# Performance work log

Measured on AMD Instinct MI355X. Metric: run time of the kernel, lower is better.

## Reference

```python
import jax, jax.numpy as jnp
import numpy as np

B, S, H, UNITS = 32, 2048, 1024, 1024


def setup_inputs() -> dict:
    key = jax.random.key(0)
    ks = jax.random.split(key, 5)
    scale = 1.0 / np.sqrt(H)
    return {
        "query": jax.random.normal(ks[0], (B, H), dtype=jnp.float32),
        "values": jax.random.normal(ks[1], (B, S, H), dtype=jnp.float32),
        "W1": jax.random.normal(ks[2], (H, UNITS), dtype=jnp.float32) * scale,
        "b1": jnp.zeros((UNITS,), dtype=jnp.float32),
        "W2": jax.random.normal(ks[3], (H, UNITS), dtype=jnp.float32) * scale,
        "b2": jnp.zeros((UNITS,), dtype=jnp.float32),
        "V": jax.random.normal(ks[4], (UNITS, 1), dtype=jnp.float32) * (1.0 / np.sqrt(UNITS)),
        "bV": jnp.zeros((1,), dtype=jnp.float32),
    }


def reference(query, values, W1, b1, W2, b2, V, bV):
    # W1(values): [B,S,U]; W2(query): [B,1,U] broadcast over S
    proj_v = jnp.einsum("bsh,hu->bsu", values, W1) + b1
    proj_q = (query @ W2 + b2)[:, None, :]
    score = jnp.tanh(proj_v + proj_q) @ V + bV          # [B,S,1]
    attention_weights = jax.nn.softmax(score, axis=1)   # softmax over seq
    context_vector = jnp.sum(attention_weights * values, axis=1)  # [B,H]
    return (attention_weights, context_vector)
```

## Files before the change

kernel.cpp:

```cpp
#include <hip/hip_runtime.h>
#include <hip/hip_bf16.h>
#include <stdint.h>

#define B_ 32
#define S_ 2048
#define H_ 1024
#define U_ 1024

typedef __attribute__((ext_vector_type(8))) short short8;
typedef __attribute__((ext_vector_type(4))) float f32x4;

__device__ __forceinline__ unsigned short f2bf(float f) {
  unsigned int u = __float_as_uint(f);
  u += 0x7fffu + ((u >> 16) & 1u);
  return (unsigned short)(u >> 16);
}

__global__ void k_transpose_w1(const float* __restrict__ W1, unsigned short* __restrict__ W1T) {
  __shared__ float tile[64][65];
  const int tx = threadIdx.x, ty = threadIdx.y;
  const int u0 = blockIdx.x * 64, h0 = blockIdx.y * 64;
#pragma unroll
  for (int i = 0; i < 16; ++i) {
    int hl = ty + i * 4;
    tile[hl][tx] = W1[(size_t)(h0 + hl) * U_ + (u0 + tx)];
  }
  __syncthreads();
#pragma unroll
  for (int i = 0; i < 16; ++i) {
    int ul = ty + i * 4;
    W1T[(size_t)(u0 + ul) * H_ + (h0 + tx)] = f2bf(tile[tx][ul]);
  }
}

__global__ void k_b1q(const float* __restrict__ query, const float* __restrict__ W2,
                      const float* __restrict__ b1, const float* __restrict__ b2,
                      float* __restrict__ b1q) {
  const int b = blockIdx.y;
  const int u = blockIdx.x * 256 + threadIdx.x;
  float acc = b1[u] + b2[u];
  const float* q = query + b * H_;
#pragma unroll 8
  for (int h = 0; h < H_; ++h) acc += q[h] * W2[(size_t)h * U_ + u];
  b1q[b * U_ + u] = acc;
}

#define BM 128
#define BN 512
#define BK 32
#define NT (H_ / BK)

__global__ __launch_bounds__(512, 2)
void k_fused_score(const float* __restrict__ values, const unsigned short* __restrict__ W1T,
                   const float* __restrict__ b1q, const float* __restrict__ V,
                   float* __restrict__ score_part) {
  __shared__ __align__(16) unsigned char smem[81920];
  unsigned short* As = (unsigned short*)smem;
  unsigned short* Bs = (unsigned short*)(smem + 16384);
  float* scorebuf = (float*)smem;

  const int tid = threadIdx.x;
  const int swz = blockIdx.x;
  const int seq = (swz & 7) * 128 + (swz >> 3);
  const int bn = seq & 1;
  const int bm = seq >> 1;

  const int lane = tid & 63, wid = tid >> 6;
  const int wm = wid >> 2, wn = wid & 3;

  const int arow = tid >> 2, aq = tid & 3;
  const float* aptr = values + (size_t)(bm * BM + arow) * H_ + aq * 8;
  const int awoff = arow * 32 + ((aq ^ ((arow >> 1) & 3)) << 3);

  const int bq = (lane & 3) ^ ((lane >> 3) & 3);
  const int u0 = bn * BN;

  const int fsq = (((lane >> 4) ^ ((lane >> 1) & 3)) << 3);

  f32x4 acc[4][8];
#pragma unroll
  for (int mf = 0; mf < 4; ++mf)
#pragma unroll
    for (int nf = 0; nf < 8; ++nf) acc[mf][nf] = (f32x4){0.f, 0.f, 0.f, 0.f};

  {
    const float4* p = (const float4*)aptr;
    float4 av0 = p[0], av1 = p[1];
#pragma unroll
    for (int i = 0; i < 4; ++i) {
      const int n = (wid * 4 + i) * 16 + (lane >> 2);
      const unsigned short* src = W1T + (size_t)(u0 + n) * H_ + bq * 8;
      __builtin_amdgcn_global_load_lds((const __attribute__((address_space(1))) void*)src,
                                       (__attribute__((address_space(3))) void*)&Bs[(wid * 4 + i) * 512],
                                       16, 0, 0);
    }
    short8 w;
    w[0]=f2bf(av0.x); w[1]=f2bf(av0.y); w[2]=f2bf(av0.z); w[3]=f2bf(av0.w);
    w[4]=f2bf(av1.x); w[5]=f2bf(av1.y); w[6]=f2bf(av1.z); w[7]=f2bf(av1.w);
    *(short8*)&As[awoff] = w;
  }
  __syncthreads();

  int cur = 0;
  for (int kt = 0; kt < NT; ++kt) {
    const bool more = (kt + 1 < NT);
    float4 av0, av1;
    if (more) {
      const float4* p = (const float4*)(aptr + (kt + 1) * BK);
      av0 = p[0]; av1 = p[1];
#pragma unroll
      for (int i = 0; i < 4; ++i) {
        const int n = (wid * 4 + i) * 16 + (lane >> 2);
        const unsigned short* src = W1T + (size_t)(u0 + n) * H_ + (kt + 1) * BK + bq * 8;
        __builtin_amdgcn_global_load_lds((const __attribute__((address_space(1))) void*)src,
                                         (__attribute__((address_space(3))) void*)&Bs[(cur ^ 1) * 16384 + (wid * 4 + i) * 512],
                                         16, 0, 0);
      }
    }
    short8 af[4], bfr[8];
#pragma unroll
    for (int mf = 0; mf < 4; ++mf) {
      const int row = wm * 64 + mf * 16 + (lane & 15);
      af[mf] = *(const short8*)&As[cur * 4096 + row * 32 + fsq];
    }
#pragma unroll
    for (int nf = 0; nf < 8; ++nf) {
      const int n = wn * 128 + nf * 16 + (lane & 15);
      bfr[nf] = *(const short8*)&Bs[cur * 16384 + n * 32 + fsq];
    }
#pragma unroll
    for (int nf = 0; nf < 8; ++nf)
#pragma unroll
      for (int mf = 0; mf < 4; ++mf)
        acc[mf][nf] = __builtin_amdgcn_mfma_f32_16x16x32_bf16(af[mf], bfr[nf], acc[mf][nf], 0, 0, 0);
    if (more) {
      short8 w;
      w[0]=f2bf(av0.x); w[1]=f2bf(av0.y); w[2]=f2bf(av0.z); w[3]=f2bf(av0.w);
      w[4]=f2bf(av1.x); w[5]=f2bf(av1.y); w[6]=f2bf(av1.z); w[7]=f2bf(av1.w);
      *(short8*)&As[(cur ^ 1) * 4096 + awoff] = w;
    }
    __syncthreads();
    cur ^= 1;
  }

  const int b_blk = bm >> 4;
  float bqv[8], vv[8];
#pragma unroll
  for (int nf = 0; nf < 8; ++nf) {
    const int ug = u0 + wn * 128 + nf * 16 + (lane & 15);
    bqv[nf] = b1q[b_blk * U_ + ug];
    vv[nf] = V[ug];
  }
  float rp[4][4];
#pragma unroll
  for (int mf = 0; mf < 4; ++mf)
#pragma unroll
    for (int j = 0; j < 4; ++j) rp[mf][j] = 0.f;
#pragma unroll
  for (int nf = 0; nf < 8; ++nf)
#pragma unroll
    for (int mf = 0; mf < 4; ++mf) {
      const f32x4 c = acc[mf][nf];
#pragma unroll
      for (int j = 0; j < 4; ++j) {
        const float x = c[j] + bqv[nf];
        const float e = __expf(2.f * x);
        const float t = 1.f - 2.f / (e + 1.f);
        rp[mf][j] += t * vv[nf];
      }
    }
#pragma unroll
  for (int mf = 0; mf < 4; ++mf)
#pragma unroll
    for (int j = 0; j < 4; ++j) {
      float v = rp[mf][j];
      v += __shfl_xor(v, 1);
      v += __shfl_xor(v, 2);
      v += __shfl_xor(v, 4);
      v += __shfl_xor(v, 8);
      rp[mf][j] = v;
    }
  if ((lane & 15) == 0) {
#pragma unroll
    for (int mf = 0; mf < 4; ++mf)
#pragma unroll
      for (int j = 0; j < 4; ++j)
        scorebuf[(wm * 64 + mf * 16 + (lane >> 4) * 4 + j) * 4 + wn] = rp[mf][j];
  }
  __syncthreads();
  if (tid < BM) {
    const float s = scorebuf[tid * 4 + 0] + scorebuf[tid * 4 + 1] +
                    scorebuf[tid * 4 + 2] + scorebuf[tid * 4 + 3];
    score_part[(size_t)bn * (B_ * S_) + bm * BM + tid] = s;
  }
}

__global__ void k_softmax(const float* __restrict__ p0, const float* __restrict__ p1,
                          float* __restrict__ aw) {
  __shared__ float red[8];
  const int b = blockIdx.x, tid = threadIdx.x;
  float x[8];
  float m = -1e30f;
#pragma unroll
  for (int i = 0; i < 8; ++i) {
    const int s = tid + i * 256;
    x[i] = p0[b * S_ + s] + p1[b * S_ + s];
    m = fmaxf(m, x[i]);
  }
#pragma unroll
  for (int off = 32; off; off >>= 1) m = fmaxf(m, __shfl_xor(m, off));
  if ((tid & 63) == 0) red[tid >> 6] = m;
  __syncthreads();
  m = fmaxf(fmaxf(red[0], red[1]), fmaxf(red[2], red[3]));
  float e[8];
  float sum = 0.f;
#pragma unroll
  for (int i = 0; i < 8; ++i) { e[i] = __expf(x[i] - m); sum += e[i]; }
#pragma unroll
  for (int off = 32; off; off >>= 1) sum += __shfl_xor(sum, off);
  __syncthreads();
  if ((tid & 63) == 0) red[4 + (tid >> 6)] = sum;
  __syncthreads();
  sum = red[4] + red[5] + red[6] + red[7];
  const float inv = 1.f / sum;
#pragma unroll
  for (int i = 0; i < 8; ++i) aw[b * S_ + tid + i * 256] = e[i] * inv;
}

__global__ void k_ctx_partial(const float* __restrict__ values, const float* __restrict__ aw,
                              float* __restrict__ part) {
  __shared__ float a_s[128];
  const int b = blockIdx.y, sc = blockIdx.x, tid = threadIdx.x;
  if (tid < 128) a_s[tid] = aw[b * S_ + sc * 128 + tid];
  __syncthreads();
  const float4* vp = (const float4*)values + (size_t)(b * S_ + sc * 128) * (H_ / 4) + tid;
  float4 acc = {0.f, 0.f, 0.f, 0.f};
#pragma unroll 4
  for (int i = 0; i < 128; ++i) {
    const float4 v = vp[(size_t)i * (H_ / 4)];
    const float a = a_s[i];
    acc.x += a * v.x; acc.y += a * v.y; acc.z += a * v.z; acc.w += a * v.w;
  }
  ((float4*)part)[(size_t)(b * 16 + sc) * (H_ / 4) + tid] = acc;
}

__global__ void k_ctx_combine(const float* __restrict__ part, float* __restrict__ ctx) {
  const int b = blockIdx.x, tid = threadIdx.x;
  float4 s = {0.f, 0.f, 0.f, 0.f};
#pragma unroll
  for (int c = 0; c < 16; ++c) {
    const float4 v = ((const float4*)part)[(size_t)(b * 16 + c) * (H_ / 4) + tid];
    s.x += v.x; s.y += v.y; s.z += v.z; s.w += v.w;
  }
  ((float4*)ctx)[b * (H_ / 4) + tid] = s;
}

extern "C" void kernel_launch(void* const* d_in, const int* in_sizes, int n_in,
                              void* d_out, int out_size, void* d_ws, size_t ws_size,
                              hipStream_t stream) {
  const float* query  = (const float*)d_in[0];
  const float* values = (const float*)d_in[1];
  const float* W1     = (const float*)d_in[2];
  const float* b1     = (const float*)d_in[3];
  const float* W2     = (const float*)d_in[4];
  const float* b2     = (const float*)d_in[5];
  const float* V      = (const float*)d_in[6];

  char* ws = (char*)d_ws;
  unsigned short* W1T = (unsigned short*)ws;
  float* b1q   = (float*)(ws + 2u * 1024u * 1024u);
  float* spart = (float*)(ws + 2u * 1024u * 1024u + 128u * 1024u);
  float* cpart = (float*)(ws + 2u * 1024u * 1024u + 128u * 1024u + 512u * 1024u);

  float* aw  = (float*)d_out;
  float* ctx = aw + B_ * S_;

  hipLaunchKernelGGL(k_transpose_w1, dim3(16, 16), dim3(64, 4), 0, stream, W1, W1T);
  hipLaunchKernelGGL(k_b1q,          dim3(4, 32),  dim3(256),   0, stream, query, W2, b1, b2, b1q);
  hipLaunchKernelGGL(k_fused_score,  dim3(1024),   dim3(512),   0, stream, values, W1T, b1q, V, spart);
  hipLaunchKernelGGL(k_softmax,      dim3(32),     dim3(256),   0, stream, spart, spart + B_ * S_, aw);
  hipLaunchKernelGGL(k_ctx_partial,  dim3(16, 32), dim3(256),   0, stream, values, aw, cpart);
  hipLaunchKernelGGL(k_ctx_combine,  dim3(32),     dim3(256),   0, stream, cpart, ctx);
}
```

Measured before the change: 314.1 us.

## Rewrite fused score GEMM with 256x256x64 tiles and explicit phased pipeline

The fused score GEMM moves from 128x512x32 tiles to 256x256 tiles with K=64, and the main loop is split into four phases per tile. Each phase uses manual vmcnt/lgkmcnt waits, sched barriers, raw s_barrier and setprio to overlap global loads, bf16 conversion into LDS and MFMA issue. A new XOR swizzle is applied to the LDS layout for both operands. Because there are now four N-partitions, softmax sums four score partials, which raises redundant fp32 A reads and workspace use. LDS grows to 128KB, so the launch_bounds(512,2) target may no longer be met, reducing occupancy.

```diff
diff --git a/kernel.cpp b/kernel.cpp
--- a/kernel.cpp
+++ b/kernel.cpp
@@ -9,6 +9,12 @@
 
 typedef __attribute__((ext_vector_type(8))) short short8;
 typedef __attribute__((ext_vector_type(4))) float f32x4;
+
+#define AS1 __attribute__((address_space(1)))
+#define AS3 __attribute__((address_space(3)))
+#define FENCE __builtin_amdgcn_sched_barrier(0)
+#define VMC(n) asm volatile("s_waitcnt vmcnt(" #n ")" ::: "memory")
+#define LGKM0 asm volatile("s_waitcnt lgkmcnt(0)" ::: "memory")
 
 __device__ __forceinline__ unsigned short f2bf(float f) {
   unsigned int u = __float_as_uint(f);
@@ -45,132 +51,177 @@
   b1q[b * U_ + u] = acc;
 }
 
-#define BM 128
-#define BN 512
-#define BK 32
-#define NT (H_ / BK)
+#define BMT 256
+#define BNT 256
+#define BKT 64
+#define NTILE 16
 
 __global__ __launch_bounds__(512, 2)
 void k_fused_score(const float* __restrict__ values, const unsigned short* __restrict__ W1T,
                    const float* __restrict__ b1q, const float* __restrict__ V,
                    float* __restrict__ score_part) {
-  __shared__ __align__(16) unsigned char smem[81920];
-  unsigned short* As = (unsigned short*)smem;
-  unsigned short* Bs = (unsigned short*)(smem + 16384);
+  __shared__ __align__(16) unsigned char smem[131072];
+  unsigned short* Abuf = (unsigned short*)smem;
+  unsigned short* Bbuf = (unsigned short*)(smem + 65536);
   float* scorebuf = (float*)smem;
 
   const int tid = threadIdx.x;
-  const int swz = blockIdx.x;
-  const int seq = (swz & 7) * 128 + (swz >> 3);
-  const int bn = seq & 1;
-  const int bm = seq >> 1;
+  const int g = blockIdx.x;
+  const int seq = (g & 7) * 128 + (g >> 3);
+  const int bn = seq & 3;
+  const int bm = seq >> 2;
 
   const int lane = tid & 63, wid = tid >> 6;
   const int wm = wid >> 2, wn = wid & 3;
-
-  const int arow = tid >> 2, aq = tid & 3;
-  const float* aptr = values + (size_t)(bm * BM + arow) * H_ + aq * 8;
-  const int awoff = arow * 32 + ((aq ^ ((arow >> 1) & 3)) << 3);
-
-  const int bq = (lane & 3) ^ ((lane >> 3) & 3);
-  const int u0 = bn * BN;
-
-  const int fsq = (((lane >> 4) ^ ((lane >> 1) & 3)) << 3);
-
-  f32x4 acc[4][8];
-#pragma unroll
-  for (int mf = 0; mf < 4; ++mf)
-#pragma unroll
-    for (int nf = 0; nf < 8; ++nf) acc[mf][nf] = (f32x4){0.f, 0.f, 0.f, 0.f};
-
-  {
-    const float4* p = (const float4*)aptr;
-    float4 av0 = p[0], av1 = p[1];
-#pragma unroll
-    for (int i = 0; i < 4; ++i) {
-      const int n = (wid * 4 + i) * 16 + (lane >> 2);
-      const unsigned short* src = W1T + (size_t)(u0 + n) * H_ + bq * 8;
-      __builtin_amdgcn_global_load_lds((const __attribute__((address_space(1))) void*)src,
-                                       (__attribute__((address_space(3))) void*)&Bs[(wid * 4 + i) * 512],
-                                       16, 0, 0);
-    }
-    short8 w;
-    w[0]=f2bf(av0.x); w[1]=f2bf(av0.y); w[2]=f2bf(av0.z); w[3]=f2bf(av0.w);
-    w[4]=f2bf(av1.x); w[5]=f2bf(av1.y); w[6]=f2bf(av1.z); w[7]=f2bf(av1.w);
-    *(short8*)&As[awoff] = w;
-  }
-  __syncthreads();
-
-  int cur = 0;
-  for (int kt = 0; kt < NT; ++kt) {
-    const bool more = (kt + 1 < NT);
-    float4 av0, av1;
-    if (more) {
-      const float4* p = (const float4*)(aptr + (kt + 1) * BK);
-      av0 = p[0]; av1 = p[1];
-#pragma unroll
-      for (int i = 0; i < 4; ++i) {
-        const int n = (wid * 4 + i) * 16 + (lane >> 2);
-        const unsigned short* src = W1T + (size_t)(u0 + n) * H_ + (kt + 1) * BK + bq * 8;
-        __builtin_amdgcn_global_load_lds((const __attribute__((address_space(1))) void*)src,
-                                         (__attribute__((address_space(3))) void*)&Bs[(cur ^ 1) * 16384 + (wid * 4 + i) * 512],
-                                         16, 0, 0);
-      }
-    }
-    short8 af[4], bfr[8];
-#pragma unroll
-    for (int mf = 0; mf < 4; ++mf) {
-      const int row = wm * 64 + mf * 16 + (lane & 15);
-      af[mf] = *(const short8*)&As[cur * 4096 + row * 32 + fsq];
-    }
-#pragma unroll
-    for (int nf = 0; nf < 8; ++nf) {
-      const int n = wn * 128 + nf * 16 + (lane & 15);
-      bfr[nf] = *(const short8*)&Bs[cur * 16384 + n * 32 + fsq];
-    }
-#pragma unroll
-    for (int nf = 0; nf < 8; ++nf)
-#pragma unroll
-      for (int mf = 0; mf < 4; ++mf)
-        acc[mf][nf] = __builtin_amdgcn_mfma_f32_16x16x32_bf16(af[mf], bfr[nf], acc[mf][nf], 0, 0, 0);
-    if (more) {
-      short8 w;
-      w[0]=f2bf(av0.x); w[1]=f2bf(av0.y); w[2]=f2bf(av0.z); w[3]=f2bf(av0.w);
-      w[4]=f2bf(av1.x); w[5]=f2bf(av1.y); w[6]=f2bf(av1.z); w[7]=f2bf(av1.w);
-      *(short8*)&As[(cur ^ 1) * 4096 + awoff] = w;
-    }
-    __syncthreads();
-    cur ^= 1;
-  }
-
-  const int b_blk = bm >> 4;
-  float bqv[8], vv[8];
-#pragma unroll
-  for (int nf = 0; nf < 8; ++nf) {
-    const int ug = u0 + wn * 128 + nf * 16 + (lane & 15);
+  const int u0 = bn * BNT;
+
+  const int arow = tid >> 2;
+  const int acp  = (tid & 3) * 2;
+  const float* aBase = values + (size_t)(bm * BMT) * H_;
+
+  const int l15 = lane & 15, l16 = lane >> 4, l7 = lane & 7;
+  const int pA0 = (wm * 128 + l15) * 64 + ((0 + l16) ^ l7) * 8;
+  const int pA1 = (wm * 128 + l15) * 64 + ((4 + l16) ^ l7) * 8;
+  const int pB0 = (wn * 64 + l15) * 64 + ((0 + l16) ^ l7) * 8;
+  const int pB1 = (wn * 64 + l15) * 64 + ((4 + l16) ^ l7) * 8;
+
+  f32x4 acc[8][4];
+#pragma unroll
+  for (int mf = 0; mf < 8; ++mf)
+#pragma unroll
+    for (int nf = 0; nf < 4; ++nf) acc[mf][nf] = (f32x4){0.f, 0.f, 0.f, 0.f};
+
+  float4 ar0[4], ar1[4];
+  short8 af[4], bfv[8];
+
+#define ISSUE_A(reg, tt, h) { \
+    const float4* ap_ = (const float4*)(aBase + (size_t)((h) * 128 + arow) * H_ + (tt) * 64 + acp * 8); \
+    reg[0] = ap_[0]; reg[1] = ap_[1]; reg[2] = ap_[2]; reg[3] = ap_[3]; }
+
+#define ISSUE_B(tt, dd, h) { \
+    _Pragma("unroll") \
+    for (int j_ = 0; j_ < 2; ++j_) { \
+      const int pbase_ = (h) * 1024 + (wid * 2 + j_) * 64; \
+      const int p_ = pbase_ + lane; \
+      const int nr_ = p_ >> 3; \
+      const int lc_ = (p_ & 7) ^ (nr_ & 7); \
+      const unsigned short* src_ = W1T + (size_t)(u0 + nr_) * H_ + (tt) * 64 + lc_ * 8; \
+      __builtin_amdgcn_global_load_lds((const AS1 void*)src_, (AS3 void*)&Bbuf[(dd) * 16384 + pbase_ * 8], 16, 0, 0); } }
+
+#define WRITE_A(reg, dd, h) { \
+    short8 w0_, w1_; \
+    w0_[0]=f2bf(reg[0].x); w0_[1]=f2bf(reg[0].y); w0_[2]=f2bf(reg[0].z); w0_[3]=f2bf(reg[0].w); \
+    w0_[4]=f2bf(reg[1].x); w0_[5]=f2bf(reg[1].y); w0_[6]=f2bf(reg[1].z); w0_[7]=f2bf(reg[1].w); \
+    w1_[0]=f2bf(reg[2].x); w1_[1]=f2bf(reg[2].y); w1_[2]=f2bf(reg[2].z); w1_[3]=f2bf(reg[2].w); \
+    w1_[4]=f2bf(reg[3].x); w1_[5]=f2bf(reg[3].y); w1_[6]=f2bf(reg[3].z); w1_[7]=f2bf(reg[3].w); \
+    const int rl_ = (h) * 128 + arow; \
+    *(short8*)&Abuf[(dd) * 16384 + rl_ * 64 + ((acp ^ (rl_ & 7)) << 3)] = w0_; \
+    *(short8*)&Abuf[(dd) * 16384 + rl_ * 64 + (((acp + 1) ^ (rl_ & 7)) << 3)] = w1_; }
+
+#define READ_AF(q) \
+    af[0] = *(const short8*)&Abuf[dA + pA0 + (2 * (q) + 0) * 1024]; \
+    af[1] = *(const short8*)&Abuf[dA + pA1 + (2 * (q) + 0) * 1024]; \
+    af[2] = *(const short8*)&Abuf[dA + pA0 + (2 * (q) + 1) * 1024]; \
+    af[3] = *(const short8*)&Abuf[dA + pA1 + (2 * (q) + 1) * 1024];
+
+#define PHASE_TAIL(q) \
+    FENCE; \
+    __builtin_amdgcn_s_barrier(); \
+    LGKM0; \
+    FENCE; \
+    __builtin_amdgcn_s_setprio(1); \
+    _Pragma("unroll") \
+    for (int nf_ = 0; nf_ < 4; ++nf_) { \
+      acc[2*(q)+0][nf_] = __builtin_amdgcn_mfma_f32_16x16x32_bf16(af[0], bfv[2*nf_+0], acc[2*(q)+0][nf_], 0, 0, 0); \
+      acc[2*(q)+0][nf_] = __builtin_amdgcn_mfma_f32_16x16x32_bf16(af[1], bfv[2*nf_+1], acc[2*(q)+0][nf_], 0, 0, 0); \
+      acc[2*(q)+1][nf_] = __builtin_amdgcn_mfma_f32_16x16x32_bf16(af[2], bfv[2*nf_+0], acc[2*(q)+1][nf_], 0, 0, 0); \
+      acc[2*(q)+1][nf_] = __builtin_amdgcn_mfma_f32_16x16x32_bf16(af[3], bfv[2*nf_+1], acc[2*(q)+1][nf_], 0, 0, 0); \
+    } \
+    __builtin_amdgcn_s_setprio(0); \
+    FENCE; \
+    __builtin_amdgcn_s_barrier();
+
+  ISSUE_A(ar0, 0, 0);
+  ISSUE_A(ar1, 0, 1);
+  ISSUE_B(0, 0, 0);
+  ISSUE_B(0, 0, 1);
+  VMC(8);  WRITE_A(ar0, 0, 0);
+  VMC(4);  WRITE_A(ar1, 0, 1);
+  FENCE;
+  ISSUE_A(ar0, 1, 0);
+  FENCE;
+  VMC(4);
+  LGKM0;
+  __builtin_amdgcn_s_barrier();
+
+  for (int t = 0; t < NTILE; ++t) {
+    const int d = t & 1, dn = d ^ 1;
+    const int n  = (t + 1 < NTILE) ? (t + 1) : (NTILE - 1);
+    const int n2 = (t + 2 < NTILE) ? (t + 2) : (NTILE - 1);
+    const int dA = d * 16384;
+    const int dB = d * 16384;
+
+    READ_AF(0);
+    bfv[0] = *(const short8*)&Bbuf[dB + pB0 + 0 * 1024];
+    bfv[1] = *(const short8*)&Bbuf[dB + pB1 + 0 * 1024];
+    bfv[2] = *(const short8*)&Bbuf[dB + pB0 + 1 * 1024];
+    bfv[3] = *(const short8*)&Bbuf[dB + pB1 + 1 * 1024];
+    bfv[4] = *(const short8*)&Bbuf[dB + pB0 + 2 * 1024];
+    bfv[5] = *(const short8*)&Bbuf[dB + pB1 + 2 * 1024];
+    bfv[6] = *(const short8*)&Bbuf[dB + pB0 + 3 * 1024];
+    bfv[7] = *(const short8*)&Bbuf[dB + pB1 + 3 * 1024];
+    ISSUE_A(ar1, n, 1);
+    ISSUE_B(n, dn, 0);
+    PHASE_TAIL(0);
+
+    READ_AF(1);
+    ISSUE_B(n, dn, 1);
+    PHASE_TAIL(1);
+
+    READ_AF(2);
+    VMC(8);
+    WRITE_A(ar0, dn, 0);
+    PHASE_TAIL(2);
+
+    READ_AF(3);
+    VMC(4);
+    WRITE_A(ar1, dn, 1);
+    FENCE;
+    ISSUE_A(ar0, n2, 0);
+    FENCE;
+    VMC(4);
+    PHASE_TAIL(3);
+  }
+
+  __syncthreads();
+  const int b_blk = bm >> 3;
+  float bqv[4], vvv[4];
+#pragma unroll
+  for (int nf = 0; nf < 4; ++nf) {
+    const int ug = u0 + wn * 64 + nf * 16 + l15;
     bqv[nf] = b1q[b_blk * U_ + ug];
-    vv[nf] = V[ug];
-  }
-  float rp[4][4];
-#pragma unroll
-  for (int mf = 0; mf < 4; ++mf)
+    vvv[nf] = V[ug];
+  }
+  float rp[8][4];
+#pragma unroll
+  for (int mf = 0; mf < 8; ++mf)
 #pragma unroll
     for (int j = 0; j < 4; ++j) rp[mf][j] = 0.f;
 #pragma unroll
-  for (int nf = 0; nf < 8; ++nf)
-#pragma unroll
-    for (int mf = 0; mf < 4; ++mf) {
+  for (int nf = 0; nf < 4; ++nf)
+#pragma unroll
+    for (int mf = 0; mf < 8; ++mf) {
       const f32x4 c = acc[mf][nf];
 #pragma unroll
       for (int j = 0; j < 4; ++j) {
         const float x = c[j] + bqv[nf];
         const float e = __expf(2.f * x);
-        const float t = 1.f - 2.f / (e + 1.f);
-        rp[mf][j] += t * vv[nf];
+        const float tt = 1.f - 2.f / (e + 1.f);
+        rp[mf][j] += tt * vvv[nf];
       }
     }
 #pragma unroll
-  for (int mf = 0; mf < 4; ++mf)
+  for (int mf = 0; mf < 8; ++mf)
 #pragma unroll
     for (int j = 0; j < 4; ++j) {
       float v = rp[mf][j];
@@ -180,31 +231,31 @@
       v += __shfl_xor(v, 8);
       rp[mf][j] = v;
     }
-  if ((lane & 15) == 0) {
-#pragma unroll
-    for (int mf = 0; mf < 4; ++mf)
+  if (l15 == 0) {
+#pragma unroll
+    for (int mf = 0; mf < 8; ++mf)
 #pragma unroll
       for (int j = 0; j < 4; ++j)
-        scorebuf[(wm * 64 + mf * 16 + (lane >> 4) * 4 + j) * 4 + wn] = rp[mf][j];
-  }
-  __syncthreads();
-  if (tid < BM) {
+        scorebuf[(wm * 128 + mf * 16 + l16 * 4 + j) * 4 + wn] = rp[mf][j];
+  }
+  __syncthreads();
+  if (tid < BMT) {
     const float s = scorebuf[tid * 4 + 0] + scorebuf[tid * 4 + 1] +
                     scorebuf[tid * 4 + 2] + scorebuf[tid * 4 + 3];
-    score_part[(size_t)bn * (B_ * S_) + bm * BM + tid] = s;
-  }
-}
-
-__global__ void k_softmax(const float* __restrict__ p0, const float* __restrict__ p1,
-                          float* __restrict__ aw) {
+    score_part[(size_t)bn * (B_ * S_) + bm * BMT + tid] = s;
+  }
+}
+
+__global__ void k_softmax(const float* __restrict__ sp, float* __restrict__ aw) {
   __shared__ float red[8];
   const int b = blockIdx.x, tid = threadIdx.x;
+  const int BS = B_ * S_;
   float x[8];
   float m = -1e30f;
 #pragma unroll
   for (int i = 0; i < 8; ++i) {
-    const int s = tid + i * 256;
-    x[i] = p0[b * S_ + s] + p1[b * S_ + s];
+    const int s = b * S_ + tid + i * 256;
+    x[i] = sp[s] + sp[BS + s] + sp[2 * BS + s] + sp[3 * BS + s];
     m = fmaxf(m, x[i]);
   }
 #pragma unroll
@@ -270,7 +321,7 @@
   unsigned short* W1T = (unsigned short*)ws;
   float* b1q   = (float*)(ws + 2u * 1024u * 1024u);
   float* spart = (float*)(ws + 2u * 1024u * 1024u + 128u * 1024u);
-  float* cpart = (float*)(ws + 2u * 1024u * 1024u + 128u * 1024u + 512u * 1024u);
+  float* cpart = (float*)(ws + 2u * 1024u * 1024u + 128u * 1024u + 1024u * 1024u);
 
   float* aw  = (float*)d_out;
   float* ctx = aw + B_ * S_;
@@ -278,7 +329,7 @@
   hipLaunchKernelGGL(k_transpose_w1, dim3(16, 16), dim3(64, 4), 0, stream, W1, W1T);
   hipLaunchKernelGGL(k_b1q,          dim3(4, 32),  dim3(256),   0, stream, query, W2, b1, b2, b1q);
   hipLaunchKernelGGL(k_fused_score,  dim3(1024),   dim3(512),   0, stream, values, W1T, b1q, V, spart);
-  hipLaunchKernelGGL(k_softmax,      dim3(32),     dim3(256),   0, stream, spart, spart + B_ * S_, aw);
+  hipLaunchKernelGGL(k_softmax,      dim3(32),     dim3(256),   0, stream, spart, aw);
   hipLaunchKernelGGL(k_ctx_partial,  dim3(16, 32), dim3(256),   0, stream, values, aw, cpart);
   hipLaunchKernelGGL(k_ctx_combine,  dim3(32),     dim3(256),   0, stream, cpart, ctx);
 }
```

Result: slower. 343.7 us (+9.4%).

## Pre-convert values to bf16 and stream both GEMM operands via direct LDS loads

Applied to the files above, without the earlier changes.

Adds a separate pass that converts the full values tensor to bf16 in workspace, so the fused score GEMM can load A tiles with global_load_lds instead of fp32 loads plus in-register conversion. The GEMM tile shrinks to 128x256 with a 4x4 fragment accumulator per wave, LDS drops to 48KB and launch bounds target 4 blocks per CU. Score partials grow to four slices that softmax now sums. The cost is an extra read of 256MB of fp32 and a write of 128MB of bf16, traded against halving the GEMM's A-read traffic and raising occupancy; since the N-split doubles, the A tile is now fetched four times instead of twice.

```diff
diff --git a/kernel.cpp b/kernel.cpp
--- a/kernel.cpp
+++ b/kernel.cpp
@@ -10,10 +10,25 @@
 typedef __attribute__((ext_vector_type(8))) short short8;
 typedef __attribute__((ext_vector_type(4))) float f32x4;
 
+#define AS1 __attribute__((address_space(1)))
+#define AS3 __attribute__((address_space(3)))
+
 __device__ __forceinline__ unsigned short f2bf(float f) {
   unsigned int u = __float_as_uint(f);
   u += 0x7fffu + ((u >> 16) & 1u);
   return (unsigned short)(u >> 16);
+}
+
+__global__ void k_cvt(const float* __restrict__ v, unsigned short* __restrict__ o) {
+  const size_t n = (size_t)B_ * S_ * H_;
+  const size_t stride = (size_t)gridDim.x * blockDim.x * 8;
+  for (size_t i = ((size_t)blockIdx.x * blockDim.x + threadIdx.x) * 8; i < n; i += stride) {
+    float4 a = *(const float4*)(v + i), b = *(const float4*)(v + i + 4);
+    short8 w;
+    w[0]=f2bf(a.x); w[1]=f2bf(a.y); w[2]=f2bf(a.z); w[3]=f2bf(a.w);
+    w[4]=f2bf(b.x); w[5]=f2bf(b.y); w[6]=f2bf(b.z); w[7]=f2bf(b.w);
+    *(short8*)(o + i) = w;
+  }
 }
 
 __global__ void k_transpose_w1(const float* __restrict__ W1, unsigned short* __restrict__ W1T) {
@@ -46,110 +61,89 @@
 }
 
 #define BM 128
-#define BN 512
+#define BN 256
 #define BK 32
-#define NT (H_ / BK)
-
-__global__ __launch_bounds__(512, 2)
-void k_fused_score(const float* __restrict__ values, const unsigned short* __restrict__ W1T,
+#define NSTEP 32
+
+__global__ __launch_bounds__(512, 4)
+void k_fused_score(const unsigned short* __restrict__ vbf,
+                   const unsigned short* __restrict__ W1T,
                    const float* __restrict__ b1q, const float* __restrict__ V,
                    float* __restrict__ score_part) {
-  __shared__ __align__(16) unsigned char smem[81920];
+  __shared__ __align__(16) unsigned char smem[49152];
   unsigned short* As = (unsigned short*)smem;
   unsigned short* Bs = (unsigned short*)(smem + 16384);
   float* scorebuf = (float*)smem;
 
   const int tid = threadIdx.x;
-  const int swz = blockIdx.x;
-  const int seq = (swz & 7) * 128 + (swz >> 3);
-  const int bn = seq & 1;
-  const int bm = seq >> 1;
+  const int g = blockIdx.x;
+  const int seq = (g & 7) * 256 + (g >> 3);
+  const int bn = seq & 3;
+  const int bm = seq >> 2;
 
   const int lane = tid & 63, wid = tid >> 6;
   const int wm = wid >> 2, wn = wid & 3;
-
-  const int arow = tid >> 2, aq = tid & 3;
-  const float* aptr = values + (size_t)(bm * BM + arow) * H_ + aq * 8;
-  const int awoff = arow * 32 + ((aq ^ ((arow >> 1) & 3)) << 3);
-
-  const int bq = (lane & 3) ^ ((lane >> 3) & 3);
   const int u0 = bn * BN;
 
-  const int fsq = (((lane >> 4) ^ ((lane >> 1) & 3)) << 3);
-
-  f32x4 acc[4][8];
+  const int arow_s = tid >> 2;
+  const int alc = (tid & 3) ^ ((arow_s >> 1) & 3);
+  const unsigned short* aSrc = vbf + (size_t)(bm * BM + arow_s) * H_ + alc * 8;
+  const unsigned short* bSrc0 = W1T + (size_t)(u0 + arow_s) * H_ + alc * 8;
+  const unsigned short* bSrc1 = bSrc0 + (size_t)128 * H_;
+
+  const int l15 = lane & 15, l16 = lane >> 4;
+  const int fsq = ((l16 ^ ((lane >> 1) & 3)) << 3);
+  const int pA = (wm * 64 + l15) * 32 + fsq;
+  const int pB = (wn * 64 + l15) * 32 + fsq;
+
+  f32x4 acc[4][4];
 #pragma unroll
   for (int mf = 0; mf < 4; ++mf)
 #pragma unroll
-    for (int nf = 0; nf < 8; ++nf) acc[mf][nf] = (f32x4){0.f, 0.f, 0.f, 0.f};
-
-  {
-    const float4* p = (const float4*)aptr;
-    float4 av0 = p[0], av1 = p[1];
-#pragma unroll
-    for (int i = 0; i < 4; ++i) {
-      const int n = (wid * 4 + i) * 16 + (lane >> 2);
-      const unsigned short* src = W1T + (size_t)(u0 + n) * H_ + bq * 8;
-      __builtin_amdgcn_global_load_lds((const __attribute__((address_space(1))) void*)src,
-                                       (__attribute__((address_space(3))) void*)&Bs[(wid * 4 + i) * 512],
-                                       16, 0, 0);
+    for (int nf = 0; nf < 4; ++nf) acc[mf][nf] = (f32x4){0.f, 0.f, 0.f, 0.f};
+
+  __builtin_amdgcn_global_load_lds((const AS1 void*)aSrc,
+                                   (AS3 void*)&As[tid * 8], 16, 0, 0);
+  __builtin_amdgcn_global_load_lds((const AS1 void*)bSrc0,
+                                   (AS3 void*)&Bs[tid * 8], 16, 0, 0);
+  __builtin_amdgcn_global_load_lds((const AS1 void*)bSrc1,
+                                   (AS3 void*)&Bs[4096 + tid * 8], 16, 0, 0);
+  __syncthreads();
+
+  int cur = 0;
+  for (int t = 0; t < NSTEP; ++t) {
+    if (t + 1 < NSTEP) {
+      const int ko = (t + 1) * BK;
+      __builtin_amdgcn_global_load_lds((const AS1 void*)(aSrc + ko),
+                                       (AS3 void*)&As[(cur ^ 1) * 4096 + tid * 8], 16, 0, 0);
+      __builtin_amdgcn_global_load_lds((const AS1 void*)(bSrc0 + ko),
+                                       (AS3 void*)&Bs[(cur ^ 1) * 8192 + tid * 8], 16, 0, 0);
+      __builtin_amdgcn_global_load_lds((const AS1 void*)(bSrc1 + ko),
+                                       (AS3 void*)&Bs[(cur ^ 1) * 8192 + 4096 + tid * 8], 16, 0, 0);
     }
-    short8 w;
-    w[0]=f2bf(av0.x); w[1]=f2bf(av0.y); w[2]=f2bf(av0.z); w[3]=f2bf(av0.w);
-    w[4]=f2bf(av1.x); w[5]=f2bf(av1.y); w[6]=f2bf(av1.z); w[7]=f2bf(av1.w);
-    *(short8*)&As[awoff] = w;
-  }
-  __syncthreads();
-
-  int cur = 0;
-  for (int kt = 0; kt < NT; ++kt) {
-    const bool more = (kt + 1 < NT);
-    float4 av0, av1;
-    if (more) {
-      const float4* p = (const float4*)(aptr + (kt + 1) * BK);
-      av0 = p[0]; av1 = p[1];
-#pragma unroll
-      for (int i = 0; i < 4; ++i) {
-        const int n = (wid * 4 + i) * 16 + (lane >> 2);
-        const unsigned short* src = W1T + (size_t)(u0 + n) * H_ + (kt + 1) * BK + bq * 8;
-        __builtin_amdgcn_global_load_lds((const __attribute__((address_space(1))) void*)src,
-                                         (__attribute__((address_space(3))) void*)&Bs[(cur ^ 1) * 16384 + (wid * 4 + i) * 512],
-                                         16, 0, 0);
-      }
-    }
-    short8 af[4], bfr[8];
-#pragma unroll
-    for (int mf = 0; mf < 4; ++mf) {
-      const int row = wm * 64 + mf * 16 + (lane & 15);
-      af[mf] = *(const short8*)&As[cur * 4096 + row * 32 + fsq];
-    }
-#pragma unroll
-    for (int nf = 0; nf < 8; ++nf) {
-      const int n = wn * 128 + nf * 16 + (lane & 15);
-      bfr[nf] = *(const short8*)&Bs[cur * 16384 + n * 32 + fsq];
-    }
-#pragma unroll
-    for (int nf = 0; nf < 8; ++nf)
+    short8 af[4], bv[4];
+#pragma unroll
+    for (int mf = 0; mf < 4; ++mf)
+      af[mf] = *(const short8*)&As[cur * 4096 + pA + mf * 512];
+#pragma unroll
+    for (int nf = 0; nf < 4; ++nf)
+      bv[nf] = *(const short8*)&Bs[cur * 8192 + pB + nf * 512];
+#pragma unroll
+    for (int nf = 0; nf < 4; ++nf)
 #pragma unroll
       for (int mf = 0; mf < 4; ++mf)
-        acc[mf][nf] = __builtin_amdgcn_mfma_f32_16x16x32_bf16(af[mf], bfr[nf], acc[mf][nf], 0, 0, 0);
-    if (more) {
-      short8 w;
-      w[0]=f2bf(av0.x); w[1]=f2bf(av0.y); w[2]=f2bf(av0.z); w[3]=f2bf(av0.w);
-      w[4]=f2bf(av1.x); w[5]=f2bf(av1.y); w[6]=f2bf(av1.z); w[7]=f2bf(av1.w);
-      *(short8*)&As[(cur ^ 1) * 4096 + awoff] = w;
-    }
+        acc[mf][nf] = __builtin_amdgcn_mfma_f32_16x16x32_bf16(af[mf], bv[nf], acc[mf][nf], 0, 0, 0);
     __syncthreads();
     cur ^= 1;
   }
 
   const int b_blk = bm >> 4;
-  float bqv[8], vv[8];
-#pragma unroll
-  for (int nf = 0; nf < 8; ++nf) {
-    const int ug = u0 + wn * 128 + nf * 16 + (lane & 15);
+  float bqv[4], vvv[4];
+#pragma unroll
+  for (int nf = 0; nf < 4; ++nf) {
+    const int ug = u0 + wn * 64 + nf * 16 + l15;
     bqv[nf] = b1q[b_blk * U_ + ug];
-    vv[nf] = V[ug];
+    vvv[nf] = V[ug];
   }
   float rp[4][4];
 #pragma unroll
@@ -157,7 +151,7 @@
 #pragma unroll
     for (int j = 0; j < 4; ++j) rp[mf][j] = 0.f;
 #pragma unroll
-  for (int nf = 0; nf < 8; ++nf)
+  for (int nf = 0; nf < 4; ++nf)
 #pragma unroll
     for (int mf = 0; mf < 4; ++mf) {
       const f32x4 c = acc[mf][nf];
@@ -165,8 +159,8 @@
       for (int j = 0; j < 4; ++j) {
         const float x = c[j] + bqv[nf];
         const float e = __expf(2.f * x);
-        const float t = 1.f - 2.f / (e + 1.f);
-        rp[mf][j] += t * vv[nf];
+        const float tt = 1.f - 2.f / (e + 1.f);
+        rp[mf][j] += tt * vvv[nf];
       }
     }
 #pragma unroll
@@ -180,12 +174,12 @@
       v += __shfl_xor(v, 8);
       rp[mf][j] = v;
     }
-  if ((lane & 15) == 0) {
+  if (l15 == 0) {
 #pragma unroll
     for (int mf = 0; mf < 4; ++mf)
 #pragma unroll
       for (int j = 0; j < 4; ++j)
-        scorebuf[(wm * 64 + mf * 16 + (lane >> 4) * 4 + j) * 4 + wn] = rp[mf][j];
+        scorebuf[(wm * 64 + mf * 16 + l16 * 4 + j) * 4 + wn] = rp[mf][j];
   }
   __syncthreads();
   if (tid < BM) {
@@ -195,16 +189,16 @@
   }
 }
 
-__global__ void k_softmax(const float* __restrict__ p0, const float* __restrict__ p1,
-                          float* __restrict__ aw) {
+__global__ void k_softmax(const float* __restrict__ sp, float* __restrict__ aw) {
   __shared__ float red[8];
   const int b = blockIdx.x, tid = threadIdx.x;
+  const int BS = B_ * S_;
   float x[8];
   float m = -1e30f;
 #pragma unroll
   for (int i = 0; i < 8; ++i) {
-    const int s = tid + i * 256;
-    x[i] = p0[b * S_ + s] + p1[b * S_ + s];
+    const int s = b * S_ + tid + i * 256;
+    x[i] = sp[s] + sp[BS + s] + sp[2 * BS + s] + sp[3 * BS + s];
     m = fmaxf(m, x[i]);
   }
 #pragma unroll
@@ -270,15 +264,17 @@
   unsigned short* W1T = (unsigned short*)ws;
   float* b1q   = (float*)(ws + 2u * 1024u * 1024u);
   float* spart = (float*)(ws + 2u * 1024u * 1024u + 128u * 1024u);
-  float* cpart = (float*)(ws + 2u * 1024u * 1024u + 128u * 1024u + 512u * 1024u);
+  float* cpart = (float*)(ws + 2u * 1024u * 1024u + 128u * 1024u + 1024u * 1024u);
+  unsigned short* vbf = (unsigned short*)(ws + 8u * 1024u * 1024u);
 
   float* aw  = (float*)d_out;
   float* ctx = aw + B_ * S_;
 
-  hipLaunchKernelGGL(k_transpose_w1, dim3(16, 16), dim3(64, 4), 0, stream, W1, W1T);
-  hipLaunchKernelGGL(k_b1q,          dim3(4, 32),  dim3(256),   0, stream, query, W2, b1, b2, b1q);
-  hipLaunchKernelGGL(k_fused_score,  dim3(1024),   dim3(512),   0, stream, values, W1T, b1q, V, spart);
-  hipLaunchKernelGGL(k_softmax,      dim3(32),     dim3(256),   0, stream, spart, spart + B_ * S_, aw);
-  hipLaunchKernelGGL(k_ctx_partial,  dim3(16, 32), dim3(256),   0, stream, values, aw, cpart);
-  hipLaunchKernelGGL(k_ctx_combine,  dim3(32),     dim3(256),   0, stream, cpart, ctx);
-}
+  k_transpose_w1<<<dim3(16, 16), dim3(64, 4), 0, stream>>>(W1, W1T);
+  k_b1q<<<dim3(4, 32), dim3(256), 0, stream>>>(query, W2, b1, b2, b1q);
+  k_cvt<<<dim3(2048), dim3(256), 0, stream>>>(values, vbf);
+  k_fused_score<<<dim3(2048), dim3(512), 0, stream>>>(vbf, W1T, b1q, V, spart);
+  k_softmax<<<dim3(32), dim3(256), 0, stream>>>(spart, aw);
+  k_ctx_partial<<<dim3(16, 32), dim3(256), 0, stream>>>(values, aw, cpart);
+  k_ctx_combine<<<dim3(32), dim3(256), 0, stream>>>(cpart, ctx);
+}
```

After: 342.0 us. +8.9%, slower.
